# Kernel optimization log

Measured on AMD Instinct MI355X. Metric: run time of the kernel, lower is better.

Reference implementation:

```python
import jax, jax.numpy as jnp
import numpy as np
import math

B, N, D = 8, 2048, 64


def setup_inputs() -> dict:
    key = jax.random.key(0)
    kq, kk, kv, kd = jax.random.split(key, 4)
    Q = jax.random.normal(kq, (B, N, D), dtype=jnp.float32)
    K = jax.random.normal(kk, (B, N, D), dtype=jnp.float32)
    V = jax.random.normal(kv, (B, N, D), dtype=jnp.float32)
    dist_matrix = jax.random.uniform(kd, (N, N), dtype=jnp.float32)
    return {"Q": Q, "K": K, "V": V, "dist_matrix": dist_matrix}


def rescale_distance_matrix(dist_matrix):
    # (1 + e^1) / (1 + exp(1 - dist))
    c = 1.0
    return (c + math.e) / (c + jnp.exp(c - dist_matrix))


def reference(Q, K, V, dist_matrix):
    d_k = K.shape[-1]
    inv_sqrt_dk = 1.0 / math.sqrt(d_k)
    # [B, N, N] raw attention logits
    qk = jnp.einsum("bnd,bmd->bnm", Q, K)
    # ReLU then multiply by rescaled distance matrix [N, N] on the right
    scores = jnp.matmul(jax.nn.relu(qk), rescale_distance_matrix(dist_matrix)) * inv_sqrt_dk
    attn = jax.nn.softmax(scores, axis=-1)
    context = jnp.einsum("bnm,bmd->bnd", attn, V)
    return context
```

## Files before the change

kernel.cpp:

```cpp
#include <hip/hip_runtime.h>


typedef _Float16 f16;
typedef _Float16 f16x8 __attribute__((ext_vector_type(8)));
typedef float    f32x4 __attribute__((ext_vector_type(4)));

#define AS1C(p) ((const __attribute__((address_space(1))) void*)(p))
#define AS3(p)  ((__attribute__((address_space(3))) void*)(p))

__device__ __forceinline__ f16x8 cvt_f16x8(float4 a, float4 b){
  f16x8 v;
  v[0]=(f16)a.x; v[1]=(f16)a.y; v[2]=(f16)a.z; v[3]=(f16)a.w;
  v[4]=(f16)b.x; v[5]=(f16)b.y; v[6]=(f16)b.z; v[7]=(f16)b.w;
  return v;
}

__launch_bounds__(256, 3)
__global__ void k_qk(const float* __restrict__ Q, const float* __restrict__ Km,
                     const float* __restrict__ V, const float* __restrict__ Dm,
                     f16* __restrict__ Ph, f16* __restrict__ RhT,
                     f16* __restrict__ VhT){
  __shared__ char shm[36864];
  const int bid = blockIdx.x;
  const int t = threadIdx.x;

  if (bid >= 2048){
    f16* tl = (f16*)shm;
    const int c = t & 63, g = t >> 6;
    if (bid < 3072){
      const int pid = bid - 2048;
      const int k0 = (pid & 31)*64, m0 = (pid >> 5)*64;
#pragma unroll
      for (int i=0;i<16;++i){
        int k = g*16 + i;
        float d = Dm[(size_t)(k0 + k)*2048 + m0 + c];
        tl[k*65 + c] = (f16)(3.7182818284590452f / (1.0f + __expf(1.0f - d)));
      }
      __syncthreads();
#pragma unroll
      for (int i=0;i<16;++i){
        int m = g*16 + i;
        RhT[(size_t)(m0 + m)*2048 + k0 + c] = tl[c*65 + m];
      }
    } else {
      const int pid = bid - 3072;
      const int m0 = (pid & 31)*64, b = pid >> 5;
#pragma unroll
      for (int i=0;i<16;++i){
        int m = g*16 + i;
        tl[m*65 + c] = (f16)V[((size_t)b*2048 + m0 + m)*64 + c];
      }
      __syncthreads();
#pragma unroll
      for (int i=0;i<16;++i){
        int d = g*16 + i;
        VhT[((size_t)b*64 + d)*2048 + m0 + c] = tl[c*65 + d];
      }
    }
    return;
  }

  f16* Qt = (f16*)shm;
  f16* Kt = (f16*)(shm + 18432);
  f16* Tt = (f16*)shm;

  const int w = t>>6, l = t&63, lr = l&15, q = l>>4;
  const int m0 = (bid & 15)*128, n0 = ((bid>>4) & 15)*128, b = bid >> 8;
  const int wr = (w>>1)*64, wc = (w&1)*64;
  const float* Qb = Q  + ((size_t)b*2048 + n0)*64;
  const float* Kb = Km + ((size_t)b*2048 + m0)*64;

  const int sr = t>>3, sc = t&7;
#pragma unroll
  for (int j=0;j<4;++j){
    int row = sr + 32*j;
    const float* p  = Qb + (size_t)row*64 + sc*8;
    *(f16x8*)(Qt + row*72 + sc*8) = cvt_f16x8(*(const float4*)p, *(const float4*)(p+4));
    const float* pk = Kb + (size_t)row*64 + sc*8;
    *(f16x8*)(Kt + row*72 + sc*8) = cvt_f16x8(*(const float4*)pk, *(const float4*)(pk+4));
  }
  __syncthreads();

  f32x4 acc[4][4] = {};
#pragma unroll
  for (int kc=0;kc<2;++kc){
    f16x8 af[4], bf[4];
#pragma unroll
    for (int ti=0;ti<4;++ti) af[ti] = *(const f16x8*)(Qt + (wr+16*ti+lr)*72 + kc*32 + q*8);
#pragma unroll
    for (int tj=0;tj<4;++tj) bf[tj] = *(const f16x8*)(Kt + (wc+16*tj+lr)*72 + kc*32 + q*8);
#pragma unroll
    for (int ti=0;ti<4;++ti)
#pragma unroll
      for (int tj=0;tj<4;++tj)
        acc[ti][tj] = __builtin_amdgcn_mfma_f32_16x16x32_f16(af[ti], bf[tj], acc[ti][tj], 0,0,0);
  }
  __syncthreads();
#pragma unroll
  for (int ti=0;ti<4;++ti)
#pragma unroll
    for (int tj=0;tj<4;++tj)
#pragma unroll
      for (int r=0;r<4;++r)
        Tt[(wr+16*ti+4*q+r)*136 + wc+16*tj+lr] = (f16)(fmaxf(acc[ti][tj][r],0.f)*0.125f);
  __syncthreads();
  const int g16 = t&15, r0 = t>>4;
#pragma unroll
  for (int j=0;j<8;++j){
    int row = r0 + 16*j;
    *(f16x8*)(Ph + ((size_t)b*2048 + n0 + row)*2048 + m0 + g16*8) =
        *(const f16x8*)(Tt + row*136 + g16*8);
  }
}

__launch_bounds__(256, 2)
__global__ void k_attn(const f16* __restrict__ Ph, const f16* __restrict__ RhT,
                       const f16* __restrict__ VhT, f16* __restrict__ Op,
                       float* __restrict__ mp, float* __restrict__ lp){
  __shared__ char smem[73728];
  f16*  Pbuf = (f16*)smem;
  f16*  Rbuf = (f16*)(smem + 24576);
  f16*  El   = (f16*)smem;
  float* stat_max = (float*)(smem + 33792);
  float* stat_sum = (float*)(smem + 34816);

  const int t = threadIdx.x, w = t>>6, l = t&63, lr = l&15, q = l>>4;
  const int bid = blockIdx.x;
  const int jq = bid & 7, nbb = bid >> 3, b = nbb & 7, nb = nbb >> 3;
  const int n0 = nb*128, jg = jq*256;
  const int wc = w*64;

  const f16* Pblk = Ph  + ((size_t)b*2048 + n0)*2048;
  const f16* Vb   = VhT + (size_t)b*64*2048;

  const f16* srcP[2];
  const f16* srcR[4];
#pragma unroll
  for (int i=0;i<2;++i){
    int slot = i*256 + t, row = slot>>2, g = slot&3;
    srcP[i] = Pblk + (size_t)row*2048 + (g ^ ((row>>1)&3))*8;
  }
#pragma unroll
  for (int i=0;i<4;++i){
    int slot = i*256 + t, row = slot>>2, g = slot&3;
    srcR[i] = RhT + (size_t)(jg + row)*2048 + (g ^ ((row>>1)&3))*8;
  }

  auto stage = [&](int kc, int sb){
    const int k0 = kc*32;
#pragma unroll
    for (int i=0;i<2;++i)
      __builtin_amdgcn_global_load_lds(AS1C(srcP[i] + k0),
                                       AS3(Pbuf + sb*4096 + i*2048 + w*512), 16, 0, 0);
#pragma unroll
    for (int i=0;i<4;++i)
      __builtin_amdgcn_global_load_lds(AS1C(srcR[i] + k0),
                                       AS3(Rbuf + sb*8192 + i*2048 + w*512), 16, 0, 0);
  };

  const int swz = (lr>>1)&3;
  f32x4 acc[8][4] = {};
  f32x4 Oacc[2][2][2] = {};

  auto compute = [&](int cb){
    const f16* Pb = Pbuf + cb*4096;
    const f16* Rb = Rbuf + cb*8192;
    f16x8 bf[4];
#pragma unroll
    for (int tj=0;tj<4;++tj)
      bf[tj] = *(const f16x8*)(Rb + (wc + 16*tj + lr)*32 + (q ^ swz)*8);
    __builtin_amdgcn_s_setprio(1);
#pragma unroll
    for (int ti=0;ti<8;++ti){
      f16x8 af = *(const f16x8*)(Pb + (16*ti + lr)*32 + (q ^ swz)*8);
#pragma unroll
      for (int tj=0;tj<4;++tj)
        acc[ti][tj] = __builtin_amdgcn_mfma_f32_16x16x32_f16(af, bf[tj], acc[ti][tj], 0,0,0);
    }
    __builtin_amdgcn_s_setprio(0);
  };

  stage(0, 0);
  stage(1, 1);
  int cur = 0;
  for (int kc = 0; kc < 62; ++kc){
    asm volatile("s_waitcnt vmcnt(6)" ::: "memory");
    __builtin_amdgcn_s_barrier();
    __builtin_amdgcn_sched_barrier(0);
    int sb = cur + 2; if (sb >= 3) sb -= 3;
    stage(kc + 2, sb);
    compute(cur);
    cur += 1; if (cur >= 3) cur -= 3;
  }
  asm volatile("s_waitcnt vmcnt(6)" ::: "memory");
  __builtin_amdgcn_s_barrier();
  __builtin_amdgcn_sched_barrier(0);
  compute(cur);
  cur += 1; if (cur >= 3) cur -= 3;
  asm volatile("s_waitcnt vmcnt(0)" ::: "memory");
  __builtin_amdgcn_s_barrier();
  __builtin_amdgcn_sched_barrier(0);
  compute(cur);

  __syncthreads();

#pragma unroll
  for (int p=0;p<2;++p){
    float pm[4][4];
#pragma unroll
    for (int ti=0;ti<4;++ti)
#pragma unroll
      for (int r=0;r<4;++r)
        pm[ti][r] = fmaxf(fmaxf(acc[4*p+ti][0][r], acc[4*p+ti][1][r]),
                          fmaxf(acc[4*p+ti][2][r], acc[4*p+ti][3][r]));
#pragma unroll
    for (int mm=1;mm<16;mm<<=1)
#pragma unroll
      for (int ti=0;ti<4;++ti)
#pragma unroll
        for (int r=0;r<4;++r)
          pm[ti][r] = fmaxf(pm[ti][r], __shfl_xor(pm[ti][r], mm));
    if (lr == 0)
#pragma unroll
      for (int ti=0;ti<4;++ti)
#pragma unroll
        for (int r=0;r<4;++r)
          stat_max[(16*ti + 4*q + r)*4 + w] = pm[ti][r];
    __syncthreads();

    float Mn[4][4], ps[4][4];
#pragma unroll
    for (int ti=0;ti<4;++ti)
#pragma unroll
      for (int r=0;r<4;++r){
        int row = 16*ti + 4*q + r;
        float4 s4 = *(const float4*)&stat_max[row*4];
        Mn[ti][r] = fmaxf(fmaxf(s4.x,s4.y), fmaxf(s4.z,s4.w));
        ps[ti][r] = 0.f;
      }
#pragma unroll
    for (int ti=0;ti<4;++ti)
#pragma unroll
      for (int tj=0;tj<4;++tj)
#pragma unroll
        for (int r=0;r<4;++r){
          float e = __expf(acc[4*p+ti][tj][r] - Mn[ti][r]);
          ps[ti][r] += e;
          El[(16*ti + 4*q + r)*264 + wc + 16*tj + lr] = (f16)e;
        }
#pragma unroll
    for (int mm=1;mm<16;mm<<=1)
#pragma unroll
      for (int ti=0;ti<4;++ti)
#pragma unroll
        for (int r=0;r<4;++r)
          ps[ti][r] += __shfl_xor(ps[ti][r], mm);
    if (lr == 0)
#pragma unroll
      for (int ti=0;ti<4;++ti)
#pragma unroll
        for (int r=0;r<4;++r)
          stat_sum[(16*ti + 4*q + r)*4 + w] = ps[ti][r];
    __syncthreads();

    if (w == 0 && lr == 0)
#pragma unroll
      for (int ti=0;ti<4;++ti)
#pragma unroll
        for (int r=0;r<4;++r){
          int row = 16*ti + 4*q + r;
          float4 s4 = *(const float4*)&stat_sum[row*4];
          mp[bid*128 + 64*p + row] = Mn[ti][r];
          lp[bid*128 + 64*p + row] = s4.x + s4.y + s4.z + s4.w;
        }

    const int erb = 32*(w&1), vcb = 32*(w>>1);
#pragma unroll
    for (int ks=0; ks<8; ++ks){
      f16x8 ae[2], bv[2];
#pragma unroll
      for (int a=0;a<2;++a)
        ae[a] = *(const f16x8*)(El + (erb + 16*a + lr)*264 + ks*32 + q*8);
#pragma unroll
      for (int bb=0;bb<2;++bb)
        bv[bb] = *(const f16x8*)(Vb + (size_t)(vcb + 16*bb + lr)*2048 + jg + ks*32 + q*8);
#pragma unroll
      for (int a=0;a<2;++a)
#pragma unroll
        for (int bb=0;bb<2;++bb)
          Oacc[p][a][bb] = __builtin_amdgcn_mfma_f32_16x16x32_f16(ae[a], bv[bb], Oacc[p][a][bb], 0,0,0);
    }
    __syncthreads();
  }

#pragma unroll
  for (int p=0;p<2;++p)
#pragma unroll
    for (int a=0;a<2;++a)
#pragma unroll
      for (int bb=0;bb<2;++bb)
#pragma unroll
        for (int r=0;r<4;++r){
          int row = 64*p + 32*(w&1) + 16*a + 4*q + r;
          int col = 32*(w>>1) + 16*bb + lr;
          Op[((size_t)bid*128 + row)*64 + col] = (f16)Oacc[p][a][bb][r];
        }
}

__global__ void k_comb(const f16* __restrict__ Op, const float* __restrict__ mp,
                       const float* __restrict__ lp, float* __restrict__ out){
  const int rb = blockIdx.x >> 2;
  const int qr = blockIdx.x & 3;
  const int b = rb & 7, nb = rb >> 3;
  const int bid0 = rb << 3;
  const int t = threadIdx.x;
  const int row = qr*32 + (t >> 3);
  const int c0 = (t & 7)*8;

  float m_[8], a_[8];
  float M = -1e30f, den = 0.f;
#pragma unroll
  for (int i=0;i<8;++i){ m_[i] = mp[(bid0+i)*128 + row]; M = fmaxf(M, m_[i]); }
#pragma unroll
  for (int i=0;i<8;++i){ a_[i] = __expf(m_[i] - M); den += a_[i]*lp[(bid0+i)*128 + row]; }
  float inv = 1.0f / den;

  float o[8] = {};
#pragma unroll
  for (int i=0;i<8;++i){
    f16x8 v = *(const f16x8*)(Op + ((size_t)(bid0+i)*128 + row)*64 + c0);
#pragma unroll
    for (int e=0;e<8;++e) o[e] += a_[i]*(float)v[e];
  }
  float4 o0, o1;
  o0.x=o[0]*inv; o0.y=o[1]*inv; o0.z=o[2]*inv; o0.w=o[3]*inv;
  o1.x=o[4]*inv; o1.y=o[5]*inv; o1.z=o[6]*inv; o1.w=o[7]*inv;
  float* dst = out + ((size_t)b*2048 + nb*128 + row)*64 + c0;
  *(float4*)dst = o0;
  *(float4*)(dst+4) = o1;
}

extern "C" void kernel_launch(void* const* d_in, const int* in_sizes, int n_in,
                              void* d_out, int out_size, void* d_ws, size_t ws_size,
                              hipStream_t stream){
  (void)in_sizes; (void)n_in; (void)out_size; (void)ws_size;
  const float* Q  = (const float*)d_in[0];
  const float* K  = (const float*)d_in[1];
  const float* V  = (const float*)d_in[2];
  const float* Dm = (const float*)d_in[3];
  float* out = (float*)d_out;
  char* ws = (char*)d_ws;
  f16* Ph  = (f16*)ws;
  f16* RhT = (f16*)(ws + (size_t)64*1024*1024);
  f16* VhT = (f16*)(ws + (size_t)72*1024*1024);
  f16* Op  = (f16*)(ws + (size_t)74*1024*1024);
  float* mpp = (float*)(ws + (size_t)90*1024*1024);
  float* lpp = mpp + 1024*128;

  k_qk   <<<dim3(3328), 256, 0, stream>>>(Q, K, V, Dm, Ph, RhT, VhT);
  k_attn <<<dim3(1024), 256, 0, stream>>>(Ph, RhT, VhT, Op, mpp, lpp);
  k_comb <<<dim3(512),  256, 0, stream>>>(Op, mpp, lpp, out);
}
```

Baseline: 252.7 us.

## Enlarge attention GEMM tile to 256x256 with 8 waves and split-phase staging

```diff
diff --git a/kernel.cpp b/kernel.cpp
--- a/kernel.cpp
+++ b/kernel.cpp
@@ -20,7 +20,7 @@
                      const float* __restrict__ V, const float* __restrict__ Dm,
                      f16* __restrict__ Ph, f16* __restrict__ RhT,
                      f16* __restrict__ VhT){
-  __shared__ char shm[36864];
+  __shared__ __align__(16) char shm[36864];
   const int bid = blockIdx.x;
   const int t = threadIdx.x;
 
@@ -113,206 +113,207 @@
   }
 }
 
-__launch_bounds__(256, 2)
+__launch_bounds__(512, 2)
 __global__ void k_attn(const f16* __restrict__ Ph, const f16* __restrict__ RhT,
                        const f16* __restrict__ VhT, f16* __restrict__ Op,
                        float* __restrict__ mp, float* __restrict__ lp){
-  __shared__ char smem[73728];
-  f16*  Pbuf = (f16*)smem;
-  f16*  Rbuf = (f16*)(smem + 24576);
-  f16*  El   = (f16*)smem;
-  float* stat_max = (float*)(smem + 33792);
-  float* stat_sum = (float*)(smem + 34816);
+  __shared__ __align__(16) char smem[98304];
+  f16* As = (f16*)smem;
+  f16* Bs = (f16*)(smem + 49152);
+  f16* El = (f16*)smem;
+  float* stat_max = (float*)(smem + 67584);
+  float* stat_sum = (float*)(smem + 69632);
 
   const int t = threadIdx.x, w = t>>6, l = t&63, lr = l&15, q = l>>4;
+  const int wr = w>>2, wc2 = w&3;
   const int bid = blockIdx.x;
-  const int jq = bid & 7, nbb = bid >> 3, b = nbb & 7, nb = nbb >> 3;
-  const int n0 = nb*128, jg = jq*256;
-  const int wc = w*64;
+  const int jq = bid & 7, rbb = bid >> 3, b = rbb & 7, nb = rbb >> 3;
+  const int n0 = nb*256, jg = jq*256;
 
   const f16* Pblk = Ph  + ((size_t)b*2048 + n0)*2048;
   const f16* Vb   = VhT + (size_t)b*64*2048;
 
-  const f16* srcP[2];
-  const f16* srcR[4];
+  const f16* srcA[2];
+  const f16* srcB[2];
 #pragma unroll
   for (int i=0;i<2;++i){
-    int slot = i*256 + t, row = slot>>2, g = slot&3;
-    srcP[i] = Pblk + (size_t)row*2048 + (g ^ ((row>>1)&3))*8;
-  }
-#pragma unroll
-  for (int i=0;i<4;++i){
-    int slot = i*256 + t, row = slot>>2, g = slot&3;
-    srcR[i] = RhT + (size_t)(jg + row)*2048 + (g ^ ((row>>1)&3))*8;
-  }
-
-  auto stage = [&](int kc, int sb){
-    const int k0 = kc*32;
+    int slot = i*512 + t, row = slot>>2, g = slot&3;
+    srcA[i] = Pblk + (size_t)row*2048 + (g ^ ((row>>1)&3))*8;
+    srcB[i] = RhT + (size_t)(jg + row)*2048 + (g ^ ((row>>1)&3))*8;
+  }
+
+  auto stageA = [&](int kt, int sb){
+    const int k0 = kt*32;
 #pragma unroll
     for (int i=0;i<2;++i)
-      __builtin_amdgcn_global_load_lds(AS1C(srcP[i] + k0),
-                                       AS3(Pbuf + sb*4096 + i*2048 + w*512), 16, 0, 0);
-#pragma unroll
-    for (int i=0;i<4;++i)
-      __builtin_amdgcn_global_load_lds(AS1C(srcR[i] + k0),
-                                       AS3(Rbuf + sb*8192 + i*2048 + w*512), 16, 0, 0);
+      __builtin_amdgcn_global_load_lds(AS1C(srcA[i] + k0),
+          AS3(As + sb*8192 + i*4096 + w*512), 16, 0, 0);
+  };
+  auto stageB = [&](int kt, int sb){
+    const int k0 = kt*32;
+#pragma unroll
+    for (int i=0;i<2;++i)
+      __builtin_amdgcn_global_load_lds(AS1C(srcB[i] + k0),
+          AS3(Bs + sb*8192 + i*4096 + w*512), 16, 0, 0);
   };
 
   const int swz = (lr>>1)&3;
   f32x4 acc[8][4] = {};
-  f32x4 Oacc[2][2][2] = {};
-
-  auto compute = [&](int cb){
-    const f16* Pb = Pbuf + cb*4096;
-    const f16* Rb = Rbuf + cb*8192;
-    f16x8 bf[4];
-#pragma unroll
-    for (int tj=0;tj<4;++tj)
-      bf[tj] = *(const f16x8*)(Rb + (wc + 16*tj + lr)*32 + (q ^ swz)*8);
-    __builtin_amdgcn_s_setprio(1);
-#pragma unroll
-    for (int ti=0;ti<8;++ti){
-      f16x8 af = *(const f16x8*)(Pb + (16*ti + lr)*32 + (q ^ swz)*8);
-#pragma unroll
-      for (int tj=0;tj<4;++tj)
-        acc[ti][tj] = __builtin_amdgcn_mfma_f32_16x16x32_f16(af, bf[tj], acc[ti][tj], 0,0,0);
-    }
-    __builtin_amdgcn_s_setprio(0);
-  };
-
-  stage(0, 0);
-  stage(1, 1);
+
+  stageA(0,0); stageB(0,0);
+  stageA(1,1); stageB(1,1);
   int cur = 0;
-  for (int kc = 0; kc < 62; ++kc){
-    asm volatile("s_waitcnt vmcnt(6)" ::: "memory");
+  for (int kt = 0; kt < 64; ++kt){
+    if (kt < 63) asm volatile("s_waitcnt vmcnt(4)" ::: "memory");
+    else         asm volatile("s_waitcnt vmcnt(0)" ::: "memory");
     __builtin_amdgcn_s_barrier();
     __builtin_amdgcn_sched_barrier(0);
     int sb = cur + 2; if (sb >= 3) sb -= 3;
-    stage(kc + 2, sb);
-    compute(cur);
+    const f16* Ab = As + cur*8192;
+    const f16* Bb = Bs + cur*8192;
+
+    if (kt < 62) stageA(kt+2, sb);
+    f16x8 bf[4], af[4];
+#pragma unroll
+    for (int tj=0;tj<4;++tj)
+      bf[tj] = *(const f16x8*)(Bb + (wc2*64 + 16*tj + lr)*32 + (q^swz)*8);
+#pragma unroll
+    for (int ti=0;ti<4;++ti)
+      af[ti] = *(const f16x8*)(Ab + (wr*128 + 16*ti + lr)*32 + (q^swz)*8);
+    asm volatile("s_waitcnt lgkmcnt(0)" ::: "memory");
+    __builtin_amdgcn_sched_barrier(0);
+    __builtin_amdgcn_s_setprio(1);
+#pragma unroll
+    for (int ti=0;ti<4;++ti)
+#pragma unroll
+      for (int tj=0;tj<4;++tj)
+        acc[ti][tj] = __builtin_amdgcn_mfma_f32_16x16x32_f16(af[ti], bf[tj], acc[ti][tj], 0,0,0);
+    __builtin_amdgcn_s_setprio(0);
+    __builtin_amdgcn_s_barrier();
+    __builtin_amdgcn_sched_barrier(0);
+
+    if (kt < 62) stageB(kt+2, sb);
+#pragma unroll
+    for (int ti=0;ti<4;++ti)
+      af[ti] = *(const f16x8*)(Ab + (wr*128 + 64 + 16*ti + lr)*32 + (q^swz)*8);
+    asm volatile("s_waitcnt lgkmcnt(0)" ::: "memory");
+    __builtin_amdgcn_sched_barrier(0);
+    __builtin_amdgcn_s_setprio(1);
+#pragma unroll
+    for (int ti=0;ti<4;++ti)
+#pragma unroll
+      for (int tj=0;tj<4;++tj)
+        acc[4+ti][tj] = __builtin_amdgcn_mfma_f32_16x16x32_f16(af[ti], bf[tj], acc[4+ti][tj], 0,0,0);
+    __builtin_amdgcn_s_setprio(0);
     cur += 1; if (cur >= 3) cur -= 3;
   }
-  asm volatile("s_waitcnt vmcnt(6)" ::: "memory");
-  __builtin_amdgcn_s_barrier();
-  __builtin_amdgcn_sched_barrier(0);
-  compute(cur);
-  cur += 1; if (cur >= 3) cur -= 3;
-  asm volatile("s_waitcnt vmcnt(0)" ::: "memory");
-  __builtin_amdgcn_s_barrier();
-  __builtin_amdgcn_sched_barrier(0);
-  compute(cur);
-
   __syncthreads();
 
 #pragma unroll
   for (int p=0;p<2;++p){
-    float pm[4][4];
-#pragma unroll
-    for (int ti=0;ti<4;++ti)
-#pragma unroll
-      for (int r=0;r<4;++r)
-        pm[ti][r] = fmaxf(fmaxf(acc[4*p+ti][0][r], acc[4*p+ti][1][r]),
-                          fmaxf(acc[4*p+ti][2][r], acc[4*p+ti][3][r]));
-#pragma unroll
-    for (int mm=1;mm<16;mm<<=1)
-#pragma unroll
-      for (int ti=0;ti<4;++ti)
+    float Mn[8][4];
+    if (wr == p){
+      float pm[8][4];
+#pragma unroll
+      for (int ti=0;ti<8;++ti)
 #pragma unroll
         for (int r=0;r<4;++r)
-          pm[ti][r] = fmaxf(pm[ti][r], __shfl_xor(pm[ti][r], mm));
-    if (lr == 0)
-#pragma unroll
-      for (int ti=0;ti<4;++ti)
-#pragma unroll
-        for (int r=0;r<4;++r)
-          stat_max[(16*ti + 4*q + r)*4 + w] = pm[ti][r];
+          pm[ti][r] = fmaxf(fmaxf(acc[ti][0][r], acc[ti][1][r]),
+                            fmaxf(acc[ti][2][r], acc[ti][3][r]));
+#pragma unroll
+      for (int mm=1;mm<16;mm<<=1)
+#pragma unroll
+        for (int ti=0;ti<8;++ti)
+#pragma unroll
+          for (int r=0;r<4;++r)
+            pm[ti][r] = fmaxf(pm[ti][r], __shfl_xor(pm[ti][r], mm));
+      if (lr == 0)
+#pragma unroll
+        for (int ti=0;ti<8;++ti)
+#pragma unroll
+          for (int r=0;r<4;++r)
+            stat_max[(16*ti + 4*q + r)*4 + wc2] = pm[ti][r];
+    }
     __syncthreads();
 
-    float Mn[4][4], ps[4][4];
-#pragma unroll
-    for (int ti=0;ti<4;++ti)
-#pragma unroll
-      for (int r=0;r<4;++r){
-        int row = 16*ti + 4*q + r;
-        float4 s4 = *(const float4*)&stat_max[row*4];
-        Mn[ti][r] = fmaxf(fmaxf(s4.x,s4.y), fmaxf(s4.z,s4.w));
-        ps[ti][r] = 0.f;
-      }
-#pragma unroll
-    for (int ti=0;ti<4;++ti)
-#pragma unroll
-      for (int tj=0;tj<4;++tj)
+    if (wr == p){
+      float ps[8][4];
+#pragma unroll
+      for (int ti=0;ti<8;++ti)
 #pragma unroll
         for (int r=0;r<4;++r){
-          float e = __expf(acc[4*p+ti][tj][r] - Mn[ti][r]);
-          ps[ti][r] += e;
-          El[(16*ti + 4*q + r)*264 + wc + 16*tj + lr] = (f16)e;
+          int row = 16*ti + 4*q + r;
+          float4 s4 = *(const float4*)&stat_max[row*4];
+          Mn[ti][r] = fmaxf(fmaxf(s4.x,s4.y), fmaxf(s4.z,s4.w));
+          ps[ti][r] = 0.f;
         }
 #pragma unroll
-    for (int mm=1;mm<16;mm<<=1)
-#pragma unroll
-      for (int ti=0;ti<4;++ti)
-#pragma unroll
-        for (int r=0;r<4;++r)
-          ps[ti][r] += __shfl_xor(ps[ti][r], mm);
-    if (lr == 0)
-#pragma unroll
-      for (int ti=0;ti<4;++ti)
-#pragma unroll
-        for (int r=0;r<4;++r)
-          stat_sum[(16*ti + 4*q + r)*4 + w] = ps[ti][r];
+      for (int ti=0;ti<8;++ti)
+#pragma unroll
+        for (int tj=0;tj<4;++tj)
+#pragma unroll
+          for (int r=0;r<4;++r){
+            float e = __expf(acc[ti][tj][r] - Mn[ti][r]);
+            ps[ti][r] += e;
+            El[(16*ti + 4*q + r)*264 + wc2*64 + 16*tj + lr] = (f16)e;
+          }
+#pragma unroll
+      for (int mm=1;mm<16;mm<<=1)
+#pragma unroll
+        for (int ti=0;ti<8;++ti)
+#pragma unroll
+          for (int r=0;r<4;++r)
+            ps[ti][r] += __shfl_xor(ps[ti][r], mm);
+      if (lr == 0)
+#pragma unroll
+        for (int ti=0;ti<8;++ti)
+#pragma unroll
+          for (int r=0;r<4;++r)
+            stat_sum[(16*ti + 4*q + r)*4 + wc2] = ps[ti][r];
+    }
     __syncthreads();
 
-    if (w == 0 && lr == 0)
-#pragma unroll
-      for (int ti=0;ti<4;++ti)
+    if (wr == p && wc2 == 0 && lr == 0)
+#pragma unroll
+      for (int ti=0;ti<8;++ti)
 #pragma unroll
         for (int r=0;r<4;++r){
           int row = 16*ti + 4*q + r;
           float4 s4 = *(const float4*)&stat_sum[row*4];
-          mp[bid*128 + 64*p + row] = Mn[ti][r];
-          lp[bid*128 + 64*p + row] = s4.x + s4.y + s4.z + s4.w;
+          mp[bid*256 + p*128 + row] = Mn[ti][r];
+          lp[bid*256 + p*128 + row] = s4.x + s4.y + s4.z + s4.w;
         }
 
-    const int erb = 32*(w&1), vcb = 32*(w>>1);
-#pragma unroll
-    for (int ks=0; ks<8; ++ks){
-      f16x8 ae[2], bv[2];
-#pragma unroll
-      for (int a=0;a<2;++a)
-        ae[a] = *(const f16x8*)(El + (erb + 16*a + lr)*264 + ks*32 + q*8);
-#pragma unroll
-      for (int bb=0;bb<2;++bb)
-        bv[bb] = *(const f16x8*)(Vb + (size_t)(vcb + 16*bb + lr)*2048 + jg + ks*32 + q*8);
-#pragma unroll
-      for (int a=0;a<2;++a)
-#pragma unroll
-        for (int bb=0;bb<2;++bb)
-          Oacc[p][a][bb] = __builtin_amdgcn_mfma_f32_16x16x32_f16(ae[a], bv[bb], Oacc[p][a][bb], 0,0,0);
+    {
+      const int er0 = w*16;
+      f32x4 Ov[4] = {};
+#pragma unroll
+      for (int ks=0; ks<8; ++ks){
+        f16x8 ae = *(const f16x8*)(El + (er0 + lr)*264 + ks*32 + q*8);
+        f16x8 bv[4];
+#pragma unroll
+        for (int tj2=0;tj2<4;++tj2)
+          bv[tj2] = *(const f16x8*)(Vb + (size_t)(16*tj2 + lr)*2048 + jg + ks*32 + q*8);
+#pragma unroll
+        for (int tj2=0;tj2<4;++tj2)
+          Ov[tj2] = __builtin_amdgcn_mfma_f32_16x16x32_f16(ae, bv[tj2], Ov[tj2], 0,0,0);
+      }
+#pragma unroll
+      for (int tj2=0;tj2<4;++tj2)
+#pragma unroll
+        for (int r=0;r<4;++r)
+          Op[((size_t)bid*256 + p*128 + er0 + 4*q + r)*64 + 16*tj2 + lr] = (f16)Ov[tj2][r];
     }
     __syncthreads();
   }
-
-#pragma unroll
-  for (int p=0;p<2;++p)
-#pragma unroll
-    for (int a=0;a<2;++a)
-#pragma unroll
-      for (int bb=0;bb<2;++bb)
-#pragma unroll
-        for (int r=0;r<4;++r){
-          int row = 64*p + 32*(w&1) + 16*a + 4*q + r;
-          int col = 32*(w>>1) + 16*bb + lr;
-          Op[((size_t)bid*128 + row)*64 + col] = (f16)Oacc[p][a][bb][r];
-        }
 }
 
 __global__ void k_comb(const f16* __restrict__ Op, const float* __restrict__ mp,
                        const float* __restrict__ lp, float* __restrict__ out){
-  const int rb = blockIdx.x >> 2;
-  const int qr = blockIdx.x & 3;
-  const int b = rb & 7, nb = rb >> 3;
-  const int bid0 = rb << 3;
+  const int rbb = blockIdx.x >> 3;
+  const int qr = blockIdx.x & 7;
+  const int b = rbb & 7, nb = rbb >> 3;
+  const int bid0 = rbb << 3;
   const int t = threadIdx.x;
   const int row = qr*32 + (t >> 3);
   const int c0 = (t & 7)*8;
@@ -320,22 +321,22 @@
   float m_[8], a_[8];
   float M = -1e30f, den = 0.f;
 #pragma unroll
-  for (int i=0;i<8;++i){ m_[i] = mp[(bid0+i)*128 + row]; M = fmaxf(M, m_[i]); }
-#pragma unroll
-  for (int i=0;i<8;++i){ a_[i] = __expf(m_[i] - M); den += a_[i]*lp[(bid0+i)*128 + row]; }
+  for (int i=0;i<8;++i){ m_[i] = mp[(bid0+i)*256 + row]; M = fmaxf(M, m_[i]); }
+#pragma unroll
+  for (int i=0;i<8;++i){ a_[i] = __expf(m_[i] - M); den += a_[i]*lp[(bid0+i)*256 + row]; }
   float inv = 1.0f / den;
 
   float o[8] = {};
 #pragma unroll
   for (int i=0;i<8;++i){
-    f16x8 v = *(const f16x8*)(Op + ((size_t)(bid0+i)*128 + row)*64 + c0);
+    f16x8 v = *(const f16x8*)(Op + ((size_t)(bid0+i)*256 + row)*64 + c0);
 #pragma unroll
     for (int e=0;e<8;++e) o[e] += a_[i]*(float)v[e];
   }
   float4 o0, o1;
   o0.x=o[0]*inv; o0.y=o[1]*inv; o0.z=o[2]*inv; o0.w=o[3]*inv;
   o1.x=o[4]*inv; o1.y=o[5]*inv; o1.z=o[6]*inv; o1.w=o[7]*inv;
-  float* dst = out + ((size_t)b*2048 + nb*128 + row)*64 + c0;
+  float* dst = out + ((size_t)b*2048 + nb*256 + row)*64 + c0;
   *(float4*)dst = o0;
   *(float4*)(dst+4) = o1;
 }
@@ -355,9 +356,9 @@
   f16* VhT = (f16*)(ws + (size_t)72*1024*1024);
   f16* Op  = (f16*)(ws + (size_t)74*1024*1024);
   float* mpp = (float*)(ws + (size_t)90*1024*1024);
-  float* lpp = mpp + 1024*128;
+  float* lpp = mpp + 512*256;
 
   k_qk   <<<dim3(3328), 256, 0, stream>>>(Q, K, V, Dm, Ph, RhT, VhT);
-  k_attn <<<dim3(1024), 256, 0, stream>>>(Ph, RhT, VhT, Op, mpp, lpp);
+  k_attn <<<dim3(512),  512, 0, stream>>>(Ph, RhT, VhT, Op, mpp, lpp);
   k_comb <<<dim3(512),  256, 0, stream>>>(Op, mpp, lpp, out);
 }
```

New measurement: 300.0 us. +18.7%, slower.
